# Performance work log

Measured on AMD Instinct MI355X. Metric: run time of the kernel, lower is better.

Reference implementation:

```python
import jax, jax.numpy as jnp
import numpy as np
import math

D_MODEL = 256
N_HEADS = 4
D_HEAD = D_MODEL // N_HEADS  # 64
TT_RANK = 4
BATCH = 4
SEQ = 2048


def _xavier(key, shape):
    fan_in, fan_out = shape[0], shape[-1]
    if len(shape) == 4:  # (H, d, d, r) treated roughly like dense xavier
        fan_in, fan_out = shape[1], shape[2] * shape[3]
    lim = math.sqrt(6.0 / (fan_in + fan_out))
    return jax.random.uniform(key, shape, jnp.float32, -lim, lim)


def setup_inputs() -> dict:
    key = jax.random.key(0)
    ks = jax.random.split(key, 12)
    inp = {
        "query": jax.random.normal(ks[0], (BATCH, SEQ, D_MODEL), jnp.float32),
        "key": jax.random.normal(ks[1], (BATCH, SEQ, D_MODEL), jnp.float32),
        "value": jax.random.normal(ks[2], (BATCH, SEQ, D_MODEL), jnp.float32),
        "Wq": _xavier(ks[3], (D_MODEL, D_MODEL)),
        "bq": jnp.zeros((D_MODEL,), jnp.float32),
        "Wk": _xavier(ks[4], (D_MODEL, D_MODEL)),
        "bk": jnp.zeros((D_MODEL,), jnp.float32),
        "Wv": _xavier(ks[5], (D_MODEL, D_MODEL)),
        "bv": jnp.zeros((D_MODEL,), jnp.float32),
        "W2": _xavier(ks[6], (N_HEADS, D_HEAD, D_HEAD, TT_RANK)),
        "alpha": jnp.float32(0.5),  # nonzero so interaction path is exercised
        "Wo": _xavier(ks[7], (D_MODEL, D_MODEL)),
        "bo": jnp.zeros((D_MODEL,), jnp.float32),
    }
    return inp


def reference(query, key, value, Wq, bq, Wk, bk, Wv, bv, W2, alpha, Wo, bo):
    B, Sq, _ = query.shape
    Sk = key.shape[1]
    H, Dh = N_HEADS, D_HEAD

    # projections -> (B, H, S, Dh)
    Q = (query @ Wq + bq).reshape(B, Sq, H, Dh).transpose(0, 2, 1, 3)
    K = (key @ Wk + bk).reshape(B, Sk, H, Dh).transpose(0, 2, 1, 3)
    V = (value @ Wv + bv).reshape(B, Sk, H, Dh).transpose(0, 2, 1, 3)

    scale = math.sqrt(Dh)
    scores = jnp.einsum('bhqd,bhkd->bhqk', Q, K) / scale  # (B,H,Sq,Sk)

    # rank-2 tensor interaction: Qp[b,h,q,a,r] = sum_d Q[b,h,q,d] W2[h,d,a,r]
    #                            Kp[b,h,k,a,r] = sum_e K[b,h,k,e] W2[h,a,e,r]
    Qp = jnp.einsum('bhqd,hdar->bhqar', Q, W2)
    Kp = jnp.einsum('bhke,haer->bhkar', K, W2)
    interaction = jnp.einsum('bhqar,bhkar->bhqk', Qp, Kp) / (Dh * scale)

    total_scores = scores + alpha * interaction
    attn = jax.nn.softmax(total_scores, axis=-1)

    out = jnp.einsum('bhqk,bhkd->bhqd', attn, V)
    out = out.transpose(0, 2, 1, 3).reshape(B, Sq, H * Dh)
    return out @ Wo + bo
```

## Files before the change

kernel.cpp:

```cpp
#include <hip/hip_runtime.h>
#include <hip/hip_bf16.h>

#define BB   4
#define SS   2048
#define DM   256
#define HH   4
#define DHH  64
#define KSPL 4
#define KLEN (SS / KSPL)

typedef unsigned short ushort_t;
typedef unsigned int   uint_t;
using short8   = __attribute__((ext_vector_type(8))) short;
using ushort8  = __attribute__((ext_vector_type(8))) unsigned short;
using ushort4v = __attribute__((ext_vector_type(4))) unsigned short;
using float4v  = __attribute__((ext_vector_type(4))) float;

__device__ __forceinline__ ushort_t f2bf(float f) {
  uint_t u = __float_as_uint(f);
  uint_t r = (u + 0x7FFFu + ((u >> 16) & 1u)) >> 16;
  return (ushort_t)r;
}

__global__ __launch_bounds__(256) void k_pre(
    const float* __restrict__ Wk, const float* __restrict__ Wv,
    const float* __restrict__ Wo, const float* __restrict__ Wq,
    const float* __restrict__ bq, const float* __restrict__ W2,
    const float* __restrict__ alpha_p,
    ushort_t* __restrict__ WkT, ushort_t* __restrict__ WvT,
    ushort_t* __restrict__ WoT, ushort_t* __restrict__ WcT,
    float* __restrict__ bc) {
  __shared__ float sT[64 * 65];
  __shared__ __align__(16) float sM[64];
  const int t = threadIdx.x;
  const int bi = blockIdx.x;
  if (bi < 48) {
    int m = bi >> 4, tile = bi & 15;
    int ot = tile >> 2, ct = tile & 3;
    const float* src = (m == 0) ? Wk : (m == 1) ? Wv : Wo;
    ushort_t* dst = (m == 0) ? WkT : (m == 1) ? WvT : WoT;
#pragma unroll
    for (int it = 0; it < 16; ++it) {
      int i = it * 4 + (t >> 6), j = t & 63;
      sT[i * 65 + j] = src[(ct * 64 + i) * 256 + ot * 64 + j];
    }
    __syncthreads();
#pragma unroll
    for (int it = 0; it < 16; ++it) {
      int jj = it * 4 + (t >> 6), ii = t & 63;
      dst[(ot * 64 + jj) * 256 + ct * 64 + ii] = f2bf(sT[ii * 65 + jj]);
    }
  } else {
    int o = bi - 48;
    int h = o >> 6, e = o & 63;
    if (t < 64) {
      const float* Wd = W2 + h * 16384 + t * 256;
      const float* We = W2 + h * 16384 + e * 4;
      float s = 0.f;
#pragma unroll 8
      for (int a = 0; a < 64; ++a) {
        float4 x = *(const float4*)(Wd + a * 4);
        float4 y = *(const float4*)(We + a * 256);
        s += x.x * y.x + x.y * y.y + x.z * y.z + x.w * y.w;
      }
      sM[t] = (t == e ? 0.125f : 0.f) + alpha_p[0] * (1.f / 512.f) * s;
    }
    __syncthreads();
    const float* Wrow = Wq + t * 256 + h * 64;
    float s = 0.f;
#pragma unroll
    for (int d4 = 0; d4 < 16; ++d4) {
      float4 x = *(const float4*)(Wrow + d4 * 4);
      float4 mm = *(const float4*)(sM + d4 * 4);
      s += x.x * mm.x + x.y * mm.y + x.z * mm.z + x.w * mm.w;
    }
    WcT[o * 256 + t] = f2bf(s);
    if (t == 0) {
      float sb = 0.f;
      for (int d = 0; d < 64; ++d) sb += bq[h * 64 + d] * sM[d];
      bc[o] = sb;
    }
  }
}

template <int MODE>
__device__ __forceinline__ void pgemm(
    const ushort_t* __restrict__ sX, const ushort_t* __restrict__ WT,
    const float* __restrict__ bias, int w, int g, int l16,
    int b, int s0, ushort_t* __restrict__ dst) {
  float4v acc[2];
  acc[0] = (float4v){0.f, 0.f, 0.f, 0.f};
  acc[1] = (float4v){0.f, 0.f, 0.f, 0.f};
#pragma unroll
  for (int kc = 0; kc < 8; ++kc) {
    short8 af = *(const short8*)&sX[l16 * 256 + (((kc * 4 + g) ^ (l16 & 7)) << 3)];
#pragma unroll
    for (int ct = 0; ct < 2; ++ct) {
      int col = w * 32 + ct * 16 + l16;
      short8 bf = *(const short8*)&WT[col * 256 + kc * 32 + g * 8];
      acc[ct] = __builtin_amdgcn_mfma_f32_16x16x32_bf16(af, bf, acc[ct], 0, 0, 0);
    }
  }
#pragma unroll
  for (int ct = 0; ct < 2; ++ct) {
    int col = w * 32 + ct * 16 + l16;
    float bv = bias[col];
    int h = col >> 6, d = col & 63;
    if (MODE == 1) {
      ushort4v pk;
#pragma unroll
      for (int r = 0; r < 4; ++r) pk[r] = f2bf(acc[ct][r] + bv);
      *(ushort4v*)&dst[((size_t)(b * HH + h) * DHH + d) * SS + s0 + g * 4] = pk;
    } else {
#pragma unroll
      for (int r = 0; r < 4; ++r)
        dst[((size_t)(b * HH + h) * SS + s0 + g * 4 + r) * DHH + d] =
            f2bf(acc[ct][r] + bv);
    }
  }
}

__global__ __launch_bounds__(512) void k_proj(
    const float* __restrict__ q_in, const float* __restrict__ k_in,
    const float* __restrict__ v_in,
    const float* __restrict__ bk, const float* __restrict__ bv,
    const ushort_t* __restrict__ WcT, const ushort_t* __restrict__ WkT,
    const ushort_t* __restrict__ WvT, const float* __restrict__ bc,
    ushort_t* __restrict__ Qa, ushort_t* __restrict__ Ka,
    ushort_t* __restrict__ VTg) {
  __shared__ ushort_t sXq[16 * 256];
  __shared__ ushort_t sXk[16 * 256];
  __shared__ ushort_t sXv[16 * 256];

  const int t = threadIdx.x;
  const int w = t >> 6, lane = t & 63, g = lane >> 4, l16 = lane & 15;
  const int row0 = blockIdx.x * 16;
  const int b = row0 >> 11, s0 = row0 & (SS - 1);

  {
    int r = t >> 5, cf = (t & 31) * 8;
    int sw = r * 256 + (((cf >> 3) ^ (r & 7)) << 3);
    const float* qp = q_in + (size_t)(row0 + r) * DM + cf;
    const float* kp = k_in + (size_t)(row0 + r) * DM + cf;
    const float* vp = v_in + (size_t)(row0 + r) * DM + cf;
    float4 a0 = *(const float4*)qp, a1 = *(const float4*)(qp + 4);
    float4 b0 = *(const float4*)kp, b1 = *(const float4*)(kp + 4);
    float4 c0 = *(const float4*)vp, c1 = *(const float4*)(vp + 4);
    ushort8 uq, uk, uv;
    uq[0] = f2bf(a0.x); uq[1] = f2bf(a0.y); uq[2] = f2bf(a0.z); uq[3] = f2bf(a0.w);
    uq[4] = f2bf(a1.x); uq[5] = f2bf(a1.y); uq[6] = f2bf(a1.z); uq[7] = f2bf(a1.w);
    uk[0] = f2bf(b0.x); uk[1] = f2bf(b0.y); uk[2] = f2bf(b0.z); uk[3] = f2bf(b0.w);
    uk[4] = f2bf(b1.x); uk[5] = f2bf(b1.y); uk[6] = f2bf(b1.z); uk[7] = f2bf(b1.w);
    uv[0] = f2bf(c0.x); uv[1] = f2bf(c0.y); uv[2] = f2bf(c0.z); uv[3] = f2bf(c0.w);
    uv[4] = f2bf(c1.x); uv[5] = f2bf(c1.y); uv[6] = f2bf(c1.z); uv[7] = f2bf(c1.w);
    *(ushort8*)&sXq[sw] = uq;
    *(ushort8*)&sXk[sw] = uk;
    *(ushort8*)&sXv[sw] = uv;
  }
  __syncthreads();

  pgemm<0>(sXq, WcT, bc, w, g, l16, b, s0, Qa);
  pgemm<0>(sXk, WkT, bk, w, g, l16, b, s0, Ka);
  pgemm<1>(sXv, WvT, bv, w, g, l16, b, s0, VTg);
}

__global__ __launch_bounds__(256, 4) void k_attn(
    const ushort_t* __restrict__ Qa, const ushort_t* __restrict__ Ka,
    const ushort_t* __restrict__ VTg,
    float* __restrict__ Opart, float* __restrict__ lpart) {
  __shared__ ushort_t sKa[64 * 64];
  __shared__ ushort_t sVT[64 * 64];
  __shared__ ushort_t sPT[128 * 64];

  const int t = threadIdx.x;
  const int w = t >> 6, lane = t & 63, g = lane >> 4, l16 = lane & 15;
  const int bh = blockIdx.y;
  const int q0 = blockIdx.x * 128;
  const int ks = blockIdx.z;

  short8 qfrag[2][2];
#pragma unroll
  for (int s = 0; s < 2; ++s) {
    const ushort_t* qp =
        Qa + ((size_t)bh * SS + q0 + s * 64 + w * 16 + l16) * DHH + g * 8;
    qfrag[s][0] = *(const short8*)(qp);
    qfrag[s][1] = *(const short8*)(qp + 32);
  }

  const ushort_t* KaB = Ka + (size_t)bh * SS * DHH + (size_t)ks * KLEN * DHH;
  const ushort_t* VTB = VTg + (size_t)bh * DHH * SS + ks * KLEN;

  const int r0 = t >> 3, c0 = t & 7, r1 = r0 + 32;
  const int sw0 = r0 * 64 + ((c0 ^ (r0 & 7)) << 3);
  const int sw1 = r1 * 64 + ((c0 ^ (r1 & 7)) << 3);

  float l_run[2] = {0.f, 0.f};
  float4v oacc[2][4];
#pragma unroll
  for (int s = 0; s < 2; ++s)
#pragma unroll
    for (int dj = 0; dj < 4; ++dj) oacc[s][dj] = (float4v){0.f, 0.f, 0.f, 0.f};

  for (int kch = 0; kch < KLEN / 64; ++kch) {
    __syncthreads();
    {
      short8 k0 = *(const short8*)(KaB + (size_t)(kch * 64 + r0) * DHH + c0 * 8);
      short8 k1 = *(const short8*)(KaB + (size_t)(kch * 64 + r1) * DHH + c0 * 8);
      short8 v0 = *(const short8*)(VTB + (size_t)r0 * SS + kch * 64 + c0 * 8);
      short8 v1 = *(const short8*)(VTB + (size_t)r1 * SS + kch * 64 + c0 * 8);
      *(short8*)(sKa + sw0) = k0;
      *(short8*)(sKa + sw1) = k1;
      *(short8*)(sVT + sw0) = v0;
      *(short8*)(sVT + sw1) = v1;
    }
    __syncthreads();

    float4v sacc[2][4];
#pragma unroll
    for (int s = 0; s < 2; ++s)
#pragma unroll
      for (int kj = 0; kj < 4; ++kj)
        sacc[s][kj] = (float4v){-20.f, -20.f, -20.f, -20.f};
#pragma unroll
    for (int kc = 0; kc < 2; ++kc) {
#pragma unroll
      for (int kj = 0; kj < 4; ++kj) {
        int krow = kj * 16 + l16;
        short8 kf = *(const short8*)(sKa + krow * 64 +
                                     (((kc * 4 + g) ^ (krow & 7)) << 3));
        sacc[0][kj] = __builtin_amdgcn_mfma_f32_16x16x32_bf16(
            kf, qfrag[0][kc], sacc[0][kj], 0, 0, 0);
        sacc[1][kj] = __builtin_amdgcn_mfma_f32_16x16x32_bf16(
            kf, qfrag[1][kc], sacc[1][kj], 0, 0, 0);
      }
    }

#pragma unroll
    for (int s = 0; s < 2; ++s) {
      int qrow = s * 64 + w * 16 + l16;
      float lp = 0.f;
#pragma unroll
      for (int kj = 0; kj < 4; ++kj) {
        float p0 = __expf(sacc[s][kj][0]);
        float p1 = __expf(sacc[s][kj][1]);
        float p2 = __expf(sacc[s][kj][2]);
        float p3 = __expf(sacc[s][kj][3]);
        uint_t u01 = __builtin_amdgcn_perm(__float_as_uint(p1),
                                           __float_as_uint(p0), 0x07060302u);
        uint_t u23 = __builtin_amdgcn_perm(__float_as_uint(p3),
                                           __float_as_uint(p2), 0x07060302u);
        lp += __uint_as_float(__float_as_uint(p0) & 0xFFFF0000u);
        lp += __uint_as_float(__float_as_uint(p1) & 0xFFFF0000u);
        lp += __uint_as_float(__float_as_uint(p2) & 0xFFFF0000u);
        lp += __uint_as_float(__float_as_uint(p3) & 0xFFFF0000u);
        int kbase = kj * 16 + g * 4;
        uint2 pack; pack.x = u01; pack.y = u23;
        *(uint2*)(sPT + qrow * 64 + (((kbase >> 3) ^ (qrow & 7)) << 3) +
                  (kbase & 7)) = pack;
      }
      l_run[s] += lp;
    }

#pragma unroll
    for (int ck = 0; ck < 2; ++ck) {
      short8 vb[4];
#pragma unroll
      for (int dj = 0; dj < 4; ++dj) {
        int vrow = dj * 16 + l16;
        vb[dj] = *(const short8*)(sVT + vrow * 64 +
                                  (((ck * 4 + g) ^ (vrow & 7)) << 3));
      }
#pragma unroll
      for (int s = 0; s < 2; ++s) {
        int qrow = s * 64 + w * 16 + l16;
        short8 pa = *(const short8*)(sPT + qrow * 64 +
                                     (((ck * 4 + g) ^ (qrow & 7)) << 3));
#pragma unroll
        for (int dj = 0; dj < 4; ++dj)
          oacc[s][dj] = __builtin_amdgcn_mfma_f32_16x16x32_bf16(
              pa, vb[dj], oacc[s][dj], 0, 0, 0);
      }
    }
  }

  const int b = bh >> 2, h = bh & 3;
  float* Ob = Opart + (size_t)ks * (8192 * 256);
#pragma unroll
  for (int s = 0; s < 2; ++s) {
    l_run[s] += __shfl_xor(l_run[s], 16, 64);
    l_run[s] += __shfl_xor(l_run[s], 32, 64);
    if (g == 0)
      lpart[(size_t)ks * (8192 * 4) +
            ((size_t)b * SS + q0 + s * 64 + w * 16 + l16) * 4 + h] = l_run[s];
#pragma unroll
    for (int r = 0; r < 4; ++r) {
      size_t row = (size_t)b * SS + q0 + s * 64 + w * 16 + g * 4 + r;
#pragma unroll
      for (int dj = 0; dj < 4; ++dj)
        Ob[row * DM + h * DHH + dj * 16 + l16] = oacc[s][dj][r];
    }
  }
}

__global__ __launch_bounds__(512) void k_out(
    const float* __restrict__ Opart, const float* __restrict__ lpart,
    const ushort_t* __restrict__ WoT, const float* __restrict__ bo,
    float* __restrict__ Out) {
  __shared__ ushort_t sA[16 * 256];
  const int t = threadIdx.x;
  const int w = t >> 6, lane = t & 63, g = lane >> 4, l16 = lane & 15;
  const int row0 = blockIdx.x * 16;
  {
    int r = t >> 5, cf = (t & 31) * 8;
    size_t row = row0 + r;
    int h = cf >> 6;
    float l = 0.f;
    float s0 = 0.f, s1 = 0.f, s2 = 0.f, s3 = 0.f,
          s4 = 0.f, s5 = 0.f, s6 = 0.f, s7 = 0.f;
#pragma unroll
    for (int ks = 0; ks < KSPL; ++ks) {
      l += lpart[(size_t)ks * (8192 * 4) + row * 4 + h];
      const float* o = Opart + (size_t)ks * (8192 * 256) + row * DM + cf;
      float4 a0 = *(const float4*)o, a1 = *(const float4*)(o + 4);
      s0 += a0.x; s1 += a0.y; s2 += a0.z; s3 += a0.w;
      s4 += a1.x; s5 += a1.y; s6 += a1.z; s7 += a1.w;
    }
    float linv = 1.0f / l;
    ushort8 u;
    u[0] = f2bf(s0 * linv); u[1] = f2bf(s1 * linv);
    u[2] = f2bf(s2 * linv); u[3] = f2bf(s3 * linv);
    u[4] = f2bf(s4 * linv); u[5] = f2bf(s5 * linv);
    u[6] = f2bf(s6 * linv); u[7] = f2bf(s7 * linv);
    *(ushort8*)&sA[r * 256 + (((cf >> 3) ^ (r & 7)) << 3)] = u;
  }
  __syncthreads();

  float4v acc[2];
  acc[0] = (float4v){0.f, 0.f, 0.f, 0.f};
  acc[1] = (float4v){0.f, 0.f, 0.f, 0.f};
#pragma unroll
  for (int kc = 0; kc < 8; ++kc) {
    short8 af = *(const short8*)&sA[l16 * 256 + (((kc * 4 + g) ^ (l16 & 7)) << 3)];
#pragma unroll
    for (int ct = 0; ct < 2; ++ct) {
      int col = w * 32 + ct * 16 + l16;
      short8 bf = *(const short8*)&WoT[col * 256 + kc * 32 + g * 8];
      acc[ct] = __builtin_amdgcn_mfma_f32_16x16x32_bf16(af, bf, acc[ct], 0, 0, 0);
    }
  }
#pragma unroll
  for (int ct = 0; ct < 2; ++ct) {
    int col = w * 32 + ct * 16 + l16;
    float bv = bo[col];
#pragma unroll
    for (int r = 0; r < 4; ++r)
      Out[(size_t)(row0 + g * 4 + r) * DM + col] = acc[ct][r] + bv;
  }
}

extern "C" void kernel_launch(void* const* d_in, const int* in_sizes, int n_in,
                              void* d_out, int out_size, void* d_ws, size_t ws_size,
                              hipStream_t stream) {
  (void)in_sizes; (void)n_in; (void)out_size; (void)ws_size;
  const float* q_in  = (const float*)d_in[0];
  const float* k_in  = (const float*)d_in[1];
  const float* v_in  = (const float*)d_in[2];
  const float* Wq    = (const float*)d_in[3];
  const float* bq    = (const float*)d_in[4];
  const float* Wk    = (const float*)d_in[5];
  const float* bk    = (const float*)d_in[6];
  const float* Wv    = (const float*)d_in[7];
  const float* bv    = (const float*)d_in[8];
  const float* W2    = (const float*)d_in[9];
  const float* alpha = (const float*)d_in[10];
  const float* Wo    = (const float*)d_in[11];
  const float* bo    = (const float*)d_in[12];
  float* out = (float*)d_out;

  char* ws = (char*)d_ws;
  ushort_t* Qa    = (ushort_t*)ws;
  ushort_t* Ka    = (ushort_t*)(ws + 4194304);
  ushort_t* VTg   = (ushort_t*)(ws + 8388608);
  float*    Opart = (float*)(ws + 12582912);
  float*    lpart = (float*)(ws + 46137344);
  ushort_t* WkT   = (ushort_t*)(ws + 48234496);
  ushort_t* WvT   = (ushort_t*)(ws + 48365568);
  ushort_t* WoT   = (ushort_t*)(ws + 48496640);
  ushort_t* WcT   = (ushort_t*)(ws + 48627712);
  float*    bc    = (float*)(ws + 48758784);

  hipLaunchKernelGGL(k_pre, dim3(304), dim3(256), 0, stream,
                     Wk, Wv, Wo, Wq, bq, W2, alpha, WkT, WvT, WoT, WcT, bc);
  hipLaunchKernelGGL(k_proj, dim3(512), dim3(512), 0, stream,
                     q_in, k_in, v_in, bk, bv, WcT, WkT, WvT, bc, Qa, Ka, VTg);
  hipLaunchKernelGGL(k_attn, dim3(SS / 128, BB * HH, KSPL), dim3(256), 0,
                     stream, Qa, Ka, VTg, Opart, lpart);
  hipLaunchKernelGGL(k_out, dim3(512), dim3(512), 0, stream,
                     Opart, lpart, WoT, bo, out);
}
```

Measured before the change: 164.1 us.

## Restructure projection kernel: 64-row tiles per matrix, LDS-staged coalesced output stores

```diff
diff --git a/kernel.cpp b/kernel.cpp
--- a/kernel.cpp
+++ b/kernel.cpp
@@ -83,85 +83,98 @@
   }
 }
 
-template <int MODE>
-__device__ __forceinline__ void pgemm(
-    const ushort_t* __restrict__ sX, const ushort_t* __restrict__ WT,
-    const float* __restrict__ bias, int w, int g, int l16,
-    int b, int s0, ushort_t* __restrict__ dst) {
-  float4v acc[2];
-  acc[0] = (float4v){0.f, 0.f, 0.f, 0.f};
-  acc[1] = (float4v){0.f, 0.f, 0.f, 0.f};
-#pragma unroll
-  for (int kc = 0; kc < 8; ++kc) {
-    short8 af = *(const short8*)&sX[l16 * 256 + (((kc * 4 + g) ^ (l16 & 7)) << 3)];
-#pragma unroll
-    for (int ct = 0; ct < 2; ++ct) {
-      int col = w * 32 + ct * 16 + l16;
-      short8 bf = *(const short8*)&WT[col * 256 + kc * 32 + g * 8];
-      acc[ct] = __builtin_amdgcn_mfma_f32_16x16x32_bf16(af, bf, acc[ct], 0, 0, 0);
-    }
-  }
-#pragma unroll
-  for (int ct = 0; ct < 2; ++ct) {
-    int col = w * 32 + ct * 16 + l16;
-    float bv = bias[col];
-    int h = col >> 6, d = col & 63;
-    if (MODE == 1) {
-      ushort4v pk;
-#pragma unroll
-      for (int r = 0; r < 4; ++r) pk[r] = f2bf(acc[ct][r] + bv);
-      *(ushort4v*)&dst[((size_t)(b * HH + h) * DHH + d) * SS + s0 + g * 4] = pk;
-    } else {
-#pragma unroll
-      for (int r = 0; r < 4; ++r)
-        dst[((size_t)(b * HH + h) * SS + s0 + g * 4 + r) * DHH + d] =
-            f2bf(acc[ct][r] + bv);
-    }
-  }
-}
-
-__global__ __launch_bounds__(512) void k_proj(
+__global__ __launch_bounds__(256) void k_proj(
     const float* __restrict__ q_in, const float* __restrict__ k_in,
     const float* __restrict__ v_in,
-    const float* __restrict__ bk, const float* __restrict__ bv,
     const ushort_t* __restrict__ WcT, const ushort_t* __restrict__ WkT,
-    const ushort_t* __restrict__ WvT, const float* __restrict__ bc,
+    const ushort_t* __restrict__ WvT,
+    const float* __restrict__ bc, const float* __restrict__ bk,
+    const float* __restrict__ bv,
     ushort_t* __restrict__ Qa, ushort_t* __restrict__ Ka,
     ushort_t* __restrict__ VTg) {
-  __shared__ ushort_t sXq[16 * 256];
-  __shared__ ushort_t sXk[16 * 256];
-  __shared__ ushort_t sXv[16 * 256];
-
+  __shared__ ushort_t sX[64 * 256];
   const int t = threadIdx.x;
   const int w = t >> 6, lane = t & 63, g = lane >> 4, l16 = lane & 15;
-  const int row0 = blockIdx.x * 16;
+  const int m = blockIdx.y;
+  const int row0 = blockIdx.x * 64;
   const int b = row0 >> 11, s0 = row0 & (SS - 1);
-
+  const float* src = (m == 0) ? q_in : (m == 1) ? k_in : v_in;
+  const ushort_t* WT = (m == 0) ? WcT : (m == 1) ? WkT : WvT;
+  const float* bias = (m == 0) ? bc : (m == 1) ? bk : bv;
+
+#pragma unroll
+  for (int it = 0; it < 8; ++it) {
+    int blk = it * 256 + t;
+    int r = blk >> 5, c16 = blk & 31;
+    const float* p = src + (size_t)(row0 + r) * DM + c16 * 8;
+    float4 a0 = *(const float4*)p, a1 = *(const float4*)(p + 4);
+    ushort8 u;
+    u[0] = f2bf(a0.x); u[1] = f2bf(a0.y); u[2] = f2bf(a0.z); u[3] = f2bf(a0.w);
+    u[4] = f2bf(a1.x); u[5] = f2bf(a1.y); u[6] = f2bf(a1.z); u[7] = f2bf(a1.w);
+    *(ushort8*)&sX[r * 256 + ((c16 ^ (r & 7)) << 3)] = u;
+  }
+  __syncthreads();
+
+  short8 af[8];
   {
-    int r = t >> 5, cf = (t & 31) * 8;
-    int sw = r * 256 + (((cf >> 3) ^ (r & 7)) << 3);
-    const float* qp = q_in + (size_t)(row0 + r) * DM + cf;
-    const float* kp = k_in + (size_t)(row0 + r) * DM + cf;
-    const float* vp = v_in + (size_t)(row0 + r) * DM + cf;
-    float4 a0 = *(const float4*)qp, a1 = *(const float4*)(qp + 4);
-    float4 b0 = *(const float4*)kp, b1 = *(const float4*)(kp + 4);
-    float4 c0 = *(const float4*)vp, c1 = *(const float4*)(vp + 4);
-    ushort8 uq, uk, uv;
-    uq[0] = f2bf(a0.x); uq[1] = f2bf(a0.y); uq[2] = f2bf(a0.z); uq[3] = f2bf(a0.w);
-    uq[4] = f2bf(a1.x); uq[5] = f2bf(a1.y); uq[6] = f2bf(a1.z); uq[7] = f2bf(a1.w);
-    uk[0] = f2bf(b0.x); uk[1] = f2bf(b0.y); uk[2] = f2bf(b0.z); uk[3] = f2bf(b0.w);
-    uk[4] = f2bf(b1.x); uk[5] = f2bf(b1.y); uk[6] = f2bf(b1.z); uk[7] = f2bf(b1.w);
-    uv[0] = f2bf(c0.x); uv[1] = f2bf(c0.y); uv[2] = f2bf(c0.z); uv[3] = f2bf(c0.w);
-    uv[4] = f2bf(c1.x); uv[5] = f2bf(c1.y); uv[6] = f2bf(c1.z); uv[7] = f2bf(c1.w);
-    *(ushort8*)&sXq[sw] = uq;
-    *(ushort8*)&sXk[sw] = uk;
-    *(ushort8*)&sXv[sw] = uv;
+    int r = w * 16 + l16;
+#pragma unroll
+    for (int kc = 0; kc < 8; ++kc)
+      af[kc] = *(const short8*)&sX[r * 256 + (((kc * 4 + g) ^ (r & 7)) << 3)];
+  }
+
+  float4v acc[16];
+#pragma unroll
+  for (int ct = 0; ct < 16; ++ct) acc[ct] = (float4v){0.f, 0.f, 0.f, 0.f};
+#pragma unroll
+  for (int ct = 0; ct < 16; ++ct) {
+#pragma unroll
+    for (int kc = 0; kc < 8; ++kc) {
+      short8 bf = *(const short8*)&WT[(ct * 16 + l16) * 256 + kc * 32 + g * 8];
+      acc[ct] = __builtin_amdgcn_mfma_f32_16x16x32_bf16(af[kc], bf, acc[ct],
+                                                        0, 0, 0);
+    }
   }
   __syncthreads();
 
-  pgemm<0>(sXq, WcT, bc, w, g, l16, b, s0, Qa);
-  pgemm<0>(sXk, WkT, bk, w, g, l16, b, s0, Ka);
-  pgemm<1>(sXv, WvT, bv, w, g, l16, b, s0, VTg);
+#pragma unroll
+  for (int ct = 0; ct < 16; ++ct) {
+    int col = ct * 16 + l16;
+    float bv = bias[col];
+#pragma unroll
+    for (int r4 = 0; r4 < 4; ++r4) {
+      int row = w * 16 + g * 4 + r4;
+      sX[row * 256 + (((col >> 3) ^ (row & 7)) << 3) + (col & 7)] =
+          f2bf(acc[ct][r4] + bv);
+    }
+  }
+  __syncthreads();
+
+  if (m < 2) {
+    ushort_t* dst = (m == 0) ? Qa : Ka;
+#pragma unroll
+    for (int it = 0; it < 8; ++it) {
+      int blk = it * 256 + t;
+      int r = blk >> 5, c16 = blk & 31;
+      ushort8 u = *(const ushort8*)&sX[r * 256 + ((c16 ^ (r & 7)) << 3)];
+      int h = c16 >> 3, dh = (c16 * 8) & 63;
+      *(ushort8*)&dst[((size_t)(b * HH + h) * SS + s0 + r) * DHH + dh] = u;
+    }
+  } else {
+#pragma unroll
+    for (int it = 0; it < 8; ++it) {
+      int idx = it * 256 + t;
+      int col = idx >> 3, sblk = idx & 7;
+      ushort8 u;
+#pragma unroll
+      for (int ji = 0; ji < 8; ++ji) {
+        int row = sblk * 8 + ji;
+        u[ji] = sX[row * 256 + (((col >> 3) ^ (row & 7)) << 3) + (col & 7)];
+      }
+      int h = col >> 6, dh = col & 63;
+      *(ushort8*)&VTg[((size_t)(b * HH + h) * DHH + dh) * SS + s0 + sblk * 8] = u;
+    }
+  }
 }
 
 __global__ __launch_bounds__(256, 4) void k_attn(
@@ -391,8 +404,8 @@
 
   hipLaunchKernelGGL(k_pre, dim3(304), dim3(256), 0, stream,
                      Wk, Wv, Wo, Wq, bq, W2, alpha, WkT, WvT, WoT, WcT, bc);
-  hipLaunchKernelGGL(k_proj, dim3(512), dim3(512), 0, stream,
-                     q_in, k_in, v_in, bk, bv, WcT, WkT, WvT, bc, Qa, Ka, VTg);
+  hipLaunchKernelGGL(k_proj, dim3(128, 3), dim3(256), 0, stream,
+                     q_in, k_in, v_in, WcT, WkT, WvT, bc, bk, bv, Qa, Ka, VTg);
   hipLaunchKernelGGL(k_attn, dim3(SS / 128, BB * HH, KSPL), dim3(256), 0,
                      stream, Qa, Ka, VTg, Opart, lpart);
   hipLaunchKernelGGL(k_out, dim3(512), dim3(512), 0, stream,
```

Measured after the change: 173.7 us. +5.9%, slower.
